# Optimization experiments

Measured on AMD Instinct MI355X. Metric: run time of the kernel, lower is better.

## Reference

```python
import jax, jax.numpy as jnp
import numpy as np

N, E, G = 100000, 1600000, 512
F_IN, H = 226, 128
BN_EPS = 1e-5

def _params(key):
    ks = jax.random.split(key, 34)
    p = {}
    dims = [(F_IN, H), (H, H), (H, H), (H, H)]
    i = 0
    for l, (din, dout) in enumerate(dims, start=1):
        p[f"W{l}a"] = jax.random.normal(ks[i], (din, dout), jnp.float32) * 0.05; i += 1
        p[f"b{l}a"] = jnp.zeros((dout,), jnp.float32)
        p[f"g{l}"] = jnp.ones((dout,), jnp.float32)
        p[f"be{l}"] = jnp.zeros((dout,), jnp.float32)
        p[f"rm{l}"] = jax.random.normal(ks[i], (dout,), jnp.float32) * 0.01; i += 1
        p[f"rv{l}"] = jnp.ones((dout,), jnp.float32)
        p[f"W{l}b"] = jax.random.normal(ks[i], (dout, dout), jnp.float32) * 0.05; i += 1
        p[f"b{l}b"] = jnp.zeros((dout,), jnp.float32)
    p["Wl"] = jax.random.normal(ks[i], (H, 1), jnp.float32) * 0.05
    p["bl"] = jnp.zeros((1,), jnp.float32)
    return p

def setup_inputs() -> dict:
    key = jax.random.key(0)
    k1, k2, k3, kp = jax.random.split(key, 4)
    inp = {
        "x": jax.random.normal(k1, (N, F_IN), jnp.float32),
        "edge_index": jax.random.randint(k2, (2, E), 0, N, jnp.int64),
        "batch": jnp.sort(jax.random.randint(k3, (N,), 0, G, jnp.int64)),
    }
    inp.update(_params(kp))
    return inp

def _gin_layer(x, src, dst, Wa, ba, g, be, rm, rv, Wb, bb):
    # GINConv (eps=0): mlp(x + sum_{j in N(i)} x_j)
    agg = jax.ops.segment_sum(x[src], dst, num_segments=N)  # [N,H] scatter-add
    h = (x + agg) @ Wa + ba
    h = g * (h - rm) * jax.lax.rsqrt(rv + BN_EPS) + be  # eval-mode BatchNorm1d
    h = jax.nn.relu(h)
    h = h @ Wb + bb
    return jax.nn.relu(h)  # outer F.relu after conv

def reference(x, edge_index, batch,
              W1a, b1a, g1, be1, rm1, rv1, W1b, b1b,
              W2a, b2a, g2, be2, rm2, rv2, W2b, b2b,
              W3a, b3a, g3, be3, rm3, rv3, W3b, b3b,
              W4a, b4a, g4, be4, rm4, rv4, W4b, b4b,
              Wl, bl):
    src, dst = edge_index[0], edge_index[1]
    h = _gin_layer(x, src, dst, W1a, b1a, g1, be1, rm1, rv1, W1b, b1b)
    h = _gin_layer(h, src, dst, W2a, b2a, g2, be2, rm2, rv2, W2b, b2b)
    h = _gin_layer(h, src, dst, W3a, b3a, g3, be3, rm3, rv3, W3b, b3b)
    h = _gin_layer(h, src, dst, W4a, b4a, g4, be4, rm4, rv4, W4b, b4b)
    # global mean pool over graphs
    sums = jax.ops.segment_sum(h, batch, num_segments=G)          # [G,H]
    cnts = jax.ops.segment_sum(jnp.ones((N,), h.dtype), batch, num_segments=G)
    pooled = sums / jnp.maximum(cnts, 1.0)[:, None]
    return pooled @ Wl + bl  # [G,1]
```

## Files before the change

### kernel.cpp

```cpp
#include <hip/hip_runtime.h>

#define NN 100000
#define NE 1600000
#define NG 512
#define FIN 226
#define HD 128
#define BN_EPS 1e-5f
#define NBUK 196
#define BCAP 10016

typedef __attribute__((ext_vector_type(8))) __bf16 bf16x8;
typedef __attribute__((ext_vector_type(8))) short short8;
typedef __attribute__((ext_vector_type(8))) unsigned short ushort8;
typedef __attribute__((ext_vector_type(4))) float f32x4;
typedef __attribute__((ext_vector_type(2))) float f32x2;

#define BC(x) __builtin_bit_cast(bf16x8, x)

__device__ inline unsigned short f2bf(float v) {
  unsigned u = __builtin_bit_cast(unsigned, v);
  return (unsigned short)((u + 0x7FFFu + ((u >> 16) & 1u)) >> 16);
}
__device__ inline float bf2f(unsigned short b) {
  return __builtin_bit_cast(float, (unsigned)b << 16);
}

__global__ __launch_bounds__(256) void k_bucket(const int* __restrict__ src,
                                                const int* __restrict__ dst,
                                                int* __restrict__ gcur,
                                                unsigned* __restrict__ pairs) {
  __shared__ int sd[4096];
  __shared__ int ss[4096];
  __shared__ int sh[NBUK];
  __shared__ int sexcl[NBUK];
  __shared__ int scur[NBUK];
  __shared__ int sbase[NBUK];
  __shared__ int wsum[4];
  const int tid = threadIdx.x;
  const int i0 = blockIdx.x * 4096;
  #pragma unroll
  for (int j = 0; j < 16; ++j) {
    int e = i0 + j * 256 + tid;
    sd[j * 256 + tid] = (e < NE) ? __builtin_nontemporal_load(dst + e) : -1;
    ss[j * 256 + tid] = (e < NE) ? __builtin_nontemporal_load(src + e) : 0;
  }
  if (tid < NBUK) sh[tid] = 0;
  __syncthreads();
  #pragma unroll
  for (int j = 0; j < 16; ++j) {
    int d = sd[j * 256 + tid];
    if (d >= 0) atomicAdd(&sh[d >> 9], 1);
  }
  __syncthreads();
  {
    int v = (tid < NBUK) ? sh[tid] : 0;
    int lane = tid & 63, w = tid >> 6;
    int incl = v;
    #pragma unroll
    for (int o = 1; o < 64; o <<= 1) {
      int u = __shfl_up(incl, o);
      if (lane >= o) incl += u;
    }
    if (lane == 63) wsum[w] = incl;
    __syncthreads();
    int off = 0;
    for (int k = 0; k < w; ++k) off += wsum[k];
    if (tid < NBUK) {
      int ex = off + incl - v;
      sexcl[tid] = ex;
      scur[tid] = ex;
      sbase[tid] = (v > 0) ? atomicAdd(&gcur[tid], v) : 0;
    }
  }
  __syncthreads();
  #pragma unroll
  for (int j = 0; j < 16; ++j) {
    int d = sd[j * 256 + tid];
    if (d >= 0) {
      int b = d >> 9;
      int lp = atomicAdd(&scur[b], 1);
      unsigned pk = ((unsigned)(d & 511) << 17) | (unsigned)ss[j * 256 + tid];
      pairs[(size_t)b * BCAP + sbase[b] + (lp - sexcl[b])] = pk;
    }
  }
}

__global__ __launch_bounds__(256) void k_bscan(const int* __restrict__ gcur,
                                               int* __restrict__ bucket_base,
                                               int* __restrict__ row_ptr) {
  __shared__ int wsum[4];
  const int tid = threadIdx.x;
  int v = (tid < NBUK) ? gcur[tid] : 0;
  int lane = tid & 63, w = tid >> 6;
  int incl = v;
  #pragma unroll
  for (int o = 1; o < 64; o <<= 1) {
    int u = __shfl_up(incl, o);
    if (lane >= o) incl += u;
  }
  if (lane == 63) wsum[w] = incl;
  __syncthreads();
  int off = 0;
  for (int k = 0; k < w; ++k) off += wsum[k];
  if (tid < NBUK) bucket_base[tid] = off + incl - v;
  if (tid == 0) row_ptr[NN] = NE;
}

__global__ __launch_bounds__(256) void k_pass2(const unsigned* __restrict__ pairs,
                                               const int* __restrict__ gcur,
                                               const int* __restrict__ bucket_base,
                                               int* __restrict__ row_ptr,
                                               int* __restrict__ col_idx) {
  __shared__ unsigned spk[BCAP];
  __shared__ int h[512];
  __shared__ int cur[512];
  __shared__ int wsum[4];
  const int b = blockIdx.x;
  const int tid = threadIdx.x;
  const int cnt = gcur[b];
  const int base = bucket_base[b];
  for (int i = tid; i < cnt; i += 256) spk[i] = pairs[(size_t)b * BCAP + i];
  h[tid] = 0; h[tid + 256] = 0;
  __syncthreads();
  for (int i = tid; i < cnt; i += 256) atomicAdd(&h[spk[i] >> 17], 1);
  __syncthreads();
  int c0 = h[2 * tid], c1 = h[2 * tid + 1];
  {
    int v = c0 + c1;
    int lane = tid & 63, w = tid >> 6;
    int incl = v;
    #pragma unroll
    for (int o = 1; o < 64; o <<= 1) {
      int u = __shfl_up(incl, o);
      if (lane >= o) incl += u;
    }
    if (lane == 63) wsum[w] = incl;
    __syncthreads();
    int off = 0;
    for (int k = 0; k < w; ++k) off += wsum[k];
    int e0 = off + incl - v;
    int e1 = e0 + c0;
    int node0 = b * 512 + 2 * tid;
    if (node0 < NN) row_ptr[node0] = base + e0;
    if (node0 + 1 < NN) row_ptr[node0 + 1] = base + e1;
    cur[2 * tid] = e0;
    cur[2 * tid + 1] = e1;
  }
  __syncthreads();
  for (int i = tid; i < cnt; i += 256) {
    unsigned pk = spk[i];
    int dl = pk >> 17;
    int p = atomicAdd(&cur[dl], 1);
    col_idx[base + p] = (int)(pk & 0x1FFFFu);
  }
}

struct PrepArgs {
  const float* W[9];
  const float* g[9];
  const float* rv[9];
  unsigned short* out[9];
  int k0[9];
  int K[9];
  const float* ba[4];
  const float* gg[4];
  const float* be[4];
  const float* rm[4];
  const float* rvv[4];
  float* bout;
};

__global__ __launch_bounds__(256) void k_prep(PrepArgs a) {
  int id = blockIdx.x * 256 + threadIdx.x;
  if (id < 9 * 16384) {
    int chunk = id >> 14;
    int r = id & 16383;
    int kk = r >> 7;
    int n = r & 127;
    float s = a.g[chunk] ? a.g[chunk][n] * rsqrtf(a.rv[chunk][n] + BN_EPS) : 1.f;
    int kg = a.k0[chunk] + kk;
    float v = (kg < a.K[chunk]) ? a.W[chunk][(size_t)kg * HD + n] * s : 0.f;
    unsigned short hb = f2bf(v);
    unsigned short lb = f2bf(v - bf2f(hb));
    int idx = n * 128 + (kk ^ ((n & 7) << 3));
    a.out[chunk][idx] = hb;
    a.out[chunk][16384 + idx] = lb;
  } else {
    int t = id - 9 * 16384;
    if (t < 512) {
      int l = t >> 7, c = t & 127;
      float s = a.gg[l][c] * rsqrtf(a.rvv[l][c] + BN_EPS);
      a.bout[l * 128 + c] = a.ba[l][c] * s + a.be[l][c] - a.rm[l][c] * s;
    }
  }
}

__global__ __launch_bounds__(256) void k_mgemm1(const float* __restrict__ A,
                                                const unsigned short* __restrict__ Wz,
                                                unsigned short* __restrict__ out,
                                                int K, int nchunks) {
  __shared__ unsigned short sW[32768];
  const int tid = threadIdx.x;
  const int wv = tid >> 6, ln = tid & 63;
  const int l15 = ln & 15, l4 = ln >> 4;
  const int m0 = blockIdx.x * 128 + wv * 32;
  f32x4 acc[2][8] = {};
  const int sw = (l15 & 7) << 3;
  int kofs[4];
  #pragma unroll
  for (int ks = 0; ks < 4; ++ks) kofs[ks] = (((ks * 32 + l4 * 8) ^ sw)) + l15 * 128;

  for (int c = 0; c < nchunks; ++c) {
    {
      const ushort8* src = (const ushort8*)(Wz + (size_t)c * 32768);
      ushort8* dst = (ushort8*)sW;
      #pragma unroll
      for (int i = 0; i < 16; ++i) dst[tid + i * 256] = src[tid + i * 256];
    }
    __syncthreads();
    const int kc = c * 128;
    #pragma unroll
    for (int ks = 0; ks < 4; ++ks) {
      const int kbase = kc + ks * 32 + l4 * 8;
      const bool tail = (kc + ks * 32 + 32) > K;
      short8 ah[2], al[2];
      #pragma unroll
      for (int mf = 0; mf < 2; ++mf) {
        const int row = m0 + mf * 16 + l15;
        float v[8];
        if (row < NN && !tail) {
          const f32x2* ap = (const f32x2*)(A + (size_t)row * K + kbase);
          #pragma unroll
          for (int q = 0; q < 4; ++q) {
            f32x2 t = __builtin_nontemporal_load(ap + q);
            v[2 * q] = t[0]; v[2 * q + 1] = t[1];
          }
        } else if (row < NN) {
          #pragma unroll
          for (int j = 0; j < 8; ++j) {
            int k = kbase + j;
            v[j] = (k < K) ? A[(size_t)row * K + k] : 0.f;
          }
        } else {
          #pragma unroll
          for (int j = 0; j < 8; ++j) v[j] = 0.f;
        }
        #pragma unroll
        for (int j = 0; j < 8; ++j) {
          unsigned short hb = f2bf(v[j]);
          ah[mf][j] = (short)hb;
          al[mf][j] = (short)f2bf(v[j] - bf2f(hb));
        }
      }
      #pragma unroll
      for (int n = 0; n < 8; ++n) {
        const int idx = n * 2048 + kofs[ks];
        short8 bh = *(const short8*)&sW[idx];
        short8 bl = *(const short8*)&sW[idx + 16384];
        #pragma unroll
        for (int mf = 0; mf < 2; ++mf) {
          acc[mf][n] = __builtin_amdgcn_mfma_f32_16x16x32_bf16(BC(ah[mf]), BC(bh), acc[mf][n], 0, 0, 0);
          acc[mf][n] = __builtin_amdgcn_mfma_f32_16x16x32_bf16(BC(ah[mf]), BC(bl), acc[mf][n], 0, 0, 0);
          acc[mf][n] = __builtin_amdgcn_mfma_f32_16x16x32_bf16(BC(al[mf]), BC(bh), acc[mf][n], 0, 0, 0);
        }
      }
    }
    __syncthreads();
  }
  #pragma unroll
  for (int mf = 0; mf < 2; ++mf) {
    #pragma unroll
    for (int n = 0; n < 8; ++n) {
      const int col = n * 16 + l15;
      #pragma unroll
      for (int r = 0; r < 4; ++r) {
        const int row = m0 + mf * 16 + l4 * 4 + r;
        if (row < NN) out[(size_t)row * HD + col] = f2bf(acc[mf][n][r]);
      }
    }
  }
}

template <int BIAS, int RELU>
__global__ __launch_bounds__(256) void k_mgemmB(const unsigned short* __restrict__ A,
                                                const unsigned short* __restrict__ Wz,
                                                const float* __restrict__ bias,
                                                unsigned short* __restrict__ out) {
  __shared__ unsigned short sW[32768];
  const int tid = threadIdx.x;
  const int wv = tid >> 6, ln = tid & 63;
  const int l15 = ln & 15, l4 = ln >> 4;
  const int m0 = blockIdx.x * 128 + wv * 32;
  f32x4 acc[2][8] = {};
  const int sw = (l15 & 7) << 3;
  {
    const ushort8* src = (const ushort8*)Wz;
    ushort8* dst = (ushort8*)sW;
    #pragma unroll
    for (int i = 0; i < 16; ++i) dst[tid + i * 256] = src[tid + i * 256];
  }
  __syncthreads();
  #pragma unroll
  for (int ks = 0; ks < 4; ++ks) {
    const int kbase = ks * 32 + l4 * 8;
    short8 a[2];
    #pragma unroll
    for (int mf = 0; mf < 2; ++mf) {
      const int row = m0 + mf * 16 + l15;
      if (row < NN) a[mf] = *(const short8*)(A + (size_t)row * HD + kbase);
      else a[mf] = short8{0, 0, 0, 0, 0, 0, 0, 0};
    }
    const int kof = (kbase ^ sw) + l15 * 128;
    #pragma unroll
    for (int n = 0; n < 8; ++n) {
      const int idx = n * 2048 + kof;
      short8 bh = *(const short8*)&sW[idx];
      short8 bl = *(const short8*)&sW[idx + 16384];
      #pragma unroll
      for (int mf = 0; mf < 2; ++mf) {
        acc[mf][n] = __builtin_amdgcn_mfma_f32_16x16x32_bf16(BC(a[mf]), BC(bh), acc[mf][n], 0, 0, 0);
        acc[mf][n] = __builtin_amdgcn_mfma_f32_16x16x32_bf16(BC(a[mf]), BC(bl), acc[mf][n], 0, 0, 0);
      }
    }
  }
  #pragma unroll
  for (int mf = 0; mf < 2; ++mf) {
    #pragma unroll
    for (int n = 0; n < 8; ++n) {
      const int col = n * 16 + l15;
      float bv = BIAS ? bias[col] : 0.f;
      #pragma unroll
      for (int r = 0; r < 4; ++r) {
        const int row = m0 + mf * 16 + l4 * 4 + r;
        if (row < NN) {
          float o = acc[mf][n][r] + bv;
          if (RELU) o = fmaxf(o, 0.f);
          out[(size_t)row * HD + col] = f2bf(o);
        }
      }
    }
  }
}

__global__ __launch_bounds__(256) void k_fused(const unsigned short* __restrict__ H,
                                               const unsigned short* __restrict__ Wzb,
                                               const float* __restrict__ bb,
                                               const unsigned short* __restrict__ Wza,
                                               unsigned short* __restrict__ Yout) {
  __shared__ unsigned short sB[16384];
  __shared__ unsigned short sA2[16384];
  __shared__ unsigned short sX[8192];
  const int tid = threadIdx.x;
  const int wv = tid >> 6, ln = tid & 63;
  const int l15 = ln & 15, l4 = ln >> 4;
  const int m0 = blockIdx.x * 128 + wv * 32;
  const int sw = (l15 & 7) << 3;
  f32x4 acc2[2][8] = {};

  short8 a[2][4];
  #pragma unroll
  for (int mf = 0; mf < 2; ++mf) {
    const int row = m0 + mf * 16 + l15;
    #pragma unroll
    for (int ks = 0; ks < 4; ++ks) {
      if (row < NN) a[mf][ks] = *(const short8*)(H + (size_t)row * HD + ks * 32 + l4 * 8);
      else a[mf][ks] = short8{0, 0, 0, 0, 0, 0, 0, 0};
    }
  }

  #pragma unroll 1
  for (int p = 0; p < 2; ++p) {
    {
      ushort8* d = (ushort8*)sB;
      const ushort8* s1 = (const ushort8*)(Wzb + p * 8192);
      const ushort8* s2 = (const ushort8*)(Wzb + 16384 + p * 8192);
      #pragma unroll
      for (int i = 0; i < 4; ++i) d[tid + i * 256] = s1[tid + i * 256];
      #pragma unroll
      for (int i = 0; i < 4; ++i) d[1024 + tid + i * 256] = s2[tid + i * 256];
    }
    {
      ushort8* d2 = (ushort8*)sA2;
      const ushort8* sa = (const ushort8*)Wza;
      #pragma unroll
      for (int i = 0; i < 4; ++i) {
        int idx = tid + i * 256;
        int n = idx >> 3, q8 = idx & 7;
        d2[idx] = sa[n * 16 + p * 8 + q8];
      }
      #pragma unroll
      for (int i = 0; i < 4; ++i) {
        int idx = tid + i * 256;
        int n = idx >> 3, q8 = idx & 7;
        d2[1024 + idx] = sa[2048 + n * 16 + p * 8 + q8];
      }
    }
    __syncthreads();

    f32x4 acc1[2][4] = {};
    #pragma unroll
    for (int ks = 0; ks < 4; ++ks) {
      const int kof = (ks * 32 + l4 * 8) ^ sw;
      #pragma unroll
      for (int nf = 0; nf < 4; ++nf) {
        const int idx = (nf * 16 + l15) * 128 + kof;
        short8 bh = *(const short8*)&sB[idx];
        short8 bl = *(const short8*)&sB[8192 + idx];
        #pragma unroll
        for (int mf = 0; mf < 2; ++mf) {
          acc1[mf][nf] = __builtin_amdgcn_mfma_f32_16x16x32_bf16(BC(a[mf][ks]), BC(bh), acc1[mf][nf], 0, 0, 0);
          acc1[mf][nf] = __builtin_amdgcn_mfma_f32_16x16x32_bf16(BC(a[mf][ks]), BC(bl), acc1[mf][nf], 0, 0, 0);
        }
      }
    }
    #pragma unroll
    for (int mf = 0; mf < 2; ++mf) {
      #pragma unroll
      for (int nf = 0; nf < 4; ++nf) {
        const int colL = nf * 16 + l15;
        const float bv = bb[p * 64 + colL];
        #pragma unroll
        for (int r = 0; r < 4; ++r) {
          const int rowL = wv * 32 + mf * 16 + l4 * 4 + r;
          sX[rowL * 64 + (colL ^ ((rowL & 7) << 3))] = f2bf(fmaxf(acc1[mf][nf][r] + bv, 0.f));
        }
      }
    }
    #pragma unroll
    for (int ks2 = 0; ks2 < 2; ++ks2) {
      const int xkof = (ks2 * 32 + l4 * 8) ^ sw;
      short8 xf[2];
      #pragma unroll
      for (int mf = 0; mf < 2; ++mf) {
        const int rowL = wv * 32 + mf * 16 + l15;
        xf[mf] = *(const short8*)&sX[rowL * 64 + xkof];
      }
      #pragma unroll
      for (int nf = 0; nf < 8; ++nf) {
        const int idx = (nf * 16 + l15) * 64 + xkof;
        short8 wh = *(const short8*)&sA2[idx];
        short8 wl = *(const short8*)&sA2[8192 + idx];
        #pragma unroll
        for (int mf = 0; mf < 2; ++mf) {
          acc2[mf][nf] = __builtin_amdgcn_mfma_f32_16x16x32_bf16(BC(xf[mf]), BC(wh), acc2[mf][nf], 0, 0, 0);
          acc2[mf][nf] = __builtin_amdgcn_mfma_f32_16x16x32_bf16(BC(xf[mf]), BC(wl), acc2[mf][nf], 0, 0, 0);
        }
      }
    }
    __syncthreads();
  }
  #pragma unroll
  for (int mf = 0; mf < 2; ++mf) {
    #pragma unroll
    for (int n = 0; n < 8; ++n) {
      const int col = n * 16 + l15;
      #pragma unroll
      for (int r = 0; r < 4; ++r) {
        const int row = m0 + mf * 16 + l4 * 4 + r;
        if (row < NN) Yout[(size_t)row * HD + col] = f2bf(acc2[mf][n][r]);
      }
    }
  }
}

__global__ __launch_bounds__(256) void k_agg(const unsigned short* __restrict__ y,
                                             const int* __restrict__ row_ptr,
                                             const int* __restrict__ col_idx,
                                             const float* __restrict__ bias,
                                             unsigned short* __restrict__ h) {
  const int node = blockIdx.x * 4 + (threadIdx.x >> 6);
  const int ln = threadIdx.x & 63;
  const int l15 = ln & 15, grp = ln >> 4;
  if (node >= NN) return;
  float acc[8] = {};
  const int beg = row_ptr[node], end = row_ptr[node + 1];
  int e = beg;
  for (; e + 8 <= end; e += 8) {
    const int s0 = __builtin_nontemporal_load(col_idx + e + grp);
    const int s1 = __builtin_nontemporal_load(col_idx + e + 4 + grp);
    const ushort8 v0 = *(const ushort8*)(y + (size_t)s0 * HD + l15 * 8);
    const ushort8 v1 = *(const ushort8*)(y + (size_t)s1 * HD + l15 * 8);
    #pragma unroll
    for (int j = 0; j < 8; ++j)
      acc[j] += bf2f((unsigned short)v0[j]) + bf2f((unsigned short)v1[j]);
  }
  if (e + 4 <= end) {
    const int s0 = __builtin_nontemporal_load(col_idx + e + grp);
    const ushort8 v0 = *(const ushort8*)(y + (size_t)s0 * HD + l15 * 8);
    #pragma unroll
    for (int j = 0; j < 8; ++j) acc[j] += bf2f((unsigned short)v0[j]);
    e += 4;
  }
  if (e + grp < end) {
    const int s0 = col_idx[e + grp];
    const ushort8 v0 = *(const ushort8*)(y + (size_t)s0 * HD + l15 * 8);
    #pragma unroll
    for (int j = 0; j < 8; ++j) acc[j] += bf2f((unsigned short)v0[j]);
  }
  #pragma unroll
  for (int j = 0; j < 8; ++j) {
    acc[j] += __shfl_xor(acc[j], 16);
    acc[j] += __shfl_xor(acc[j], 32);
  }
  const ushort8 sv = *(const ushort8*)(y + (size_t)node * HD + l15 * 8);
  const f32x4* b4 = (const f32x4*)(bias + l15 * 8);
  const f32x4 b0 = b4[0], b1 = b4[1];
  ushort8 o;
  #pragma unroll
  for (int j = 0; j < 8; ++j) {
    const float bj = (j < 4) ? b0[j] : b1[j - 4];
    o[j] = (unsigned short)f2bf(fmaxf(acc[j] + bf2f((unsigned short)sv[j]) + bj, 0.f));
  }
  if (grp == 0) *(ushort8*)(h + (size_t)node * HD + l15 * 8) = o;
}

__global__ __launch_bounds__(256) void k_pool2(const unsigned short* __restrict__ h,
                                               const int* __restrict__ batch,
                                               const float* __restrict__ Wl,
                                               float* __restrict__ sums,
                                               float* __restrict__ cnts) {
  __shared__ float sb[NG];
  __shared__ int sc[NG];
  const int tid = threadIdx.x;
  for (int i = tid; i < NG; i += 256) { sb[i] = 0.f; sc[i] = 0; }
  __syncthreads();
  const int wv = tid >> 6, ln = tid & 63;
  const float2 w2 = reinterpret_cast<const float2*>(Wl)[ln];
  #pragma unroll 1
  for (int i = 0; i < 16; ++i) {
    const int node = blockIdx.x * 64 + wv * 16 + i;
    if (node < NN) {
      const ushort2 hv = reinterpret_cast<const ushort2*>(h)[(size_t)node * 64 + ln];
      float d = bf2f(hv.x) * w2.x + bf2f(hv.y) * w2.y;
      #pragma unroll
      for (int off = 32; off > 0; off >>= 1) d += __shfl_down(d, off);
      if (ln == 0) {
        const int g = batch[node];
        atomicAdd(&sb[g], d);
        atomicAdd(&sc[g], 1);
      }
    }
  }
  __syncthreads();
  for (int i = tid; i < NG; i += 256)
    if (sc[i]) { atomicAdd(&sums[i], sb[i]); atomicAdd(&cnts[i], (float)sc[i]); }
}

__global__ void k_final(const float* __restrict__ sums, const float* __restrict__ cnts,
                        const float* __restrict__ bl, float* __restrict__ out) {
  int g = blockIdx.x * 256 + threadIdx.x;
  if (g < NG) out[g] = sums[g] / fmaxf(cnts[g], 1.f) + bl[0];
}

extern "C" void kernel_launch(void* const* d_in, const int* in_sizes, int n_in,
                              void* d_out, int out_size, void* d_ws, size_t ws_size,
                              hipStream_t stream) {
  const float* x = (const float*)d_in[0];
  const int* edges = (const int*)d_in[1];
  const int* batch = (const int*)d_in[2];
  const int* e_src = edges;
  const int* e_dst = edges + NE;
  const float* Wl = (const float*)d_in[35];
  const float* bl = (const float*)d_in[36];
  float* out = (float*)d_out;
  auto P = [&](int l, int which) -> const float* {
    return (const float*)d_in[3 + (l - 1) * 8 + which];
  };

  char* ws = (char*)d_ws;
  size_t off = 0;
  auto take = [&](size_t bytes) -> void* {
    void* p = ws + off;
    off = (off + bytes + 255) & ~(size_t)255;
    return p;
  };
  unsigned short* Y = (unsigned short*)take((size_t)NN * HD * 2);
  unsigned short* H = (unsigned short*)take((size_t)NN * HD * 2);
  unsigned short* X = (unsigned short*)take((size_t)NN * HD * 2);
  int* row_ptr = (int*)take((size_t)(NN + 1) * 4);
  int* col_idx = (int*)take((size_t)NE * 4);
  unsigned* pairs = (unsigned*)take((size_t)NBUK * BCAP * 4);
  int* gcur = (int*)take((size_t)NBUK * 4);
  int* bucket_base = (int*)take((size_t)NBUK * 4);
  unsigned short* Wza[4];
  unsigned short* Wzb[4];
  Wza[0] = (unsigned short*)take((size_t)2 * 32768 * 2);
  for (int l = 1; l < 4; ++l) Wza[l] = (unsigned short*)take((size_t)32768 * 2);
  for (int l = 0; l < 4; ++l) Wzb[l] = (unsigned short*)take((size_t)32768 * 2);
  float* bf = (float*)take((size_t)4 * HD * 4);
  float* psum = (float*)take((size_t)NG * 4 * 2);
  float* pcnt = psum + NG;

  hipMemsetAsync(gcur, 0, (size_t)NBUK * 4, stream);
  k_bucket<<<(NE + 4095) / 4096, 256, 0, stream>>>(e_src, e_dst, gcur, pairs);
  k_bscan<<<1, 256, 0, stream>>>(gcur, bucket_base, row_ptr);
  k_pass2<<<NBUK, 256, 0, stream>>>(pairs, gcur, bucket_base, row_ptr, col_idx);

  PrepArgs pa;
  for (int c = 0; c < 9; ++c) {
    if (c < 2) { pa.W[c] = P(1, 0); pa.g[c] = P(1, 2); pa.rv[c] = P(1, 5);
                 pa.out[c] = Wza[0] + c * 32768; pa.k0[c] = c * 128; pa.K[c] = FIN; }
    else if (c < 5) { int l = c - 1; pa.W[c] = P(l + 1, 0); pa.g[c] = P(l + 1, 2);
                      pa.rv[c] = P(l + 1, 5); pa.out[c] = Wza[l]; pa.k0[c] = 0; pa.K[c] = HD; }
    else { int l = c - 5; pa.W[c] = P(l + 1, 6); pa.g[c] = nullptr; pa.rv[c] = nullptr;
           pa.out[c] = Wzb[l]; pa.k0[c] = 0; pa.K[c] = HD; }
  }
  for (int l = 0; l < 4; ++l) {
    pa.ba[l] = P(l + 1, 1); pa.gg[l] = P(l + 1, 2); pa.be[l] = P(l + 1, 3);
    pa.rm[l] = P(l + 1, 4); pa.rvv[l] = P(l + 1, 5);
  }
  pa.bout = bf;
  k_prep<<<(9 * 16384 + 512 + 255) / 256, 256, 0, stream>>>(pa);

  hipMemsetAsync(psum, 0, (size_t)NG * 8, stream);

  const int gemm_grid = (NN + 127) / 128;
  k_mgemm1<<<gemm_grid, 256, 0, stream>>>(x, Wza[0], Y, FIN, 2);
  for (int l = 1; l <= 3; ++l) {
    k_agg<<<NN / 4, 256, 0, stream>>>(Y, row_ptr, col_idx, bf + (l - 1) * HD, H);
    k_fused<<<gemm_grid, 256, 0, stream>>>(H, Wzb[l - 1], P(l, 7), Wza[l], Y);
  }
  k_agg<<<NN / 4, 256, 0, stream>>>(Y, row_ptr, col_idx, bf + 3 * HD, H);
  k_mgemmB<1, 1><<<gemm_grid, 256, 0, stream>>>(H, Wzb[3], P(4, 7), X);
  k_pool2<<<(NN + 63) / 64, 256, 0, stream>>>(X, batch, Wl, psum, pcnt);
  k_final<<<(NG + 255) / 256, 256, 0, stream>>>(psum, pcnt, bl, out);
}
```

Measured before the change: 533.3 us.

## Fuse neighbor aggregation into GEMM kernels and fold bucket scan into pass2

The separate aggregation kernel is merged into the per-layer fused MLP kernel. Each block gathers its 128 rows' neighbor sums into swizzled shared memory and feeds them straight to the MFMA GEMMs, so the H intermediate never goes to global memory. The last layer also fuses the second GEMM, the ReLU, the dot with Wl and the per-graph pooling into one kernel, and the bucket prefix scan is recomputed inside each pass2 block, removing two launches. The cost is that the gather is less parallel (16 lanes per row rather than a 64-thread wave split across edges), shared memory grows to about 80KB, which may lower occupancy, and Y is ping-ponged between two buffers.

```diff
diff --git a/kernel.cpp b/kernel.cpp
--- a/kernel.cpp
+++ b/kernel.cpp
@@ -85,40 +85,36 @@
   }
 }
 
-__global__ __launch_bounds__(256) void k_bscan(const int* __restrict__ gcur,
-                                               int* __restrict__ bucket_base,
-                                               int* __restrict__ row_ptr) {
-  __shared__ int wsum[4];
-  const int tid = threadIdx.x;
-  int v = (tid < NBUK) ? gcur[tid] : 0;
-  int lane = tid & 63, w = tid >> 6;
-  int incl = v;
-  #pragma unroll
-  for (int o = 1; o < 64; o <<= 1) {
-    int u = __shfl_up(incl, o);
-    if (lane >= o) incl += u;
-  }
-  if (lane == 63) wsum[w] = incl;
-  __syncthreads();
-  int off = 0;
-  for (int k = 0; k < w; ++k) off += wsum[k];
-  if (tid < NBUK) bucket_base[tid] = off + incl - v;
-  if (tid == 0) row_ptr[NN] = NE;
-}
-
 __global__ __launch_bounds__(256) void k_pass2(const unsigned* __restrict__ pairs,
                                                const int* __restrict__ gcur,
-                                               const int* __restrict__ bucket_base,
                                                int* __restrict__ row_ptr,
                                                int* __restrict__ col_idx) {
   __shared__ unsigned spk[BCAP];
   __shared__ int h[512];
   __shared__ int cur[512];
   __shared__ int wsum[4];
+  __shared__ int s_base;
   const int b = blockIdx.x;
   const int tid = threadIdx.x;
+  {
+    int v = (tid < NBUK) ? gcur[tid] : 0;
+    int lane = tid & 63, w = tid >> 6;
+    int incl = v;
+    #pragma unroll
+    for (int o = 1; o < 64; o <<= 1) {
+      int u = __shfl_up(incl, o);
+      if (lane >= o) incl += u;
+    }
+    if (lane == 63) wsum[w] = incl;
+    __syncthreads();
+    int off = 0;
+    for (int k = 0; k < w; ++k) off += wsum[k];
+    if (tid == b) s_base = off + incl - v;
+    if (b == 0 && tid == 0) row_ptr[NN] = NE;
+  }
   const int cnt = gcur[b];
-  const int base = bucket_base[b];
+  __syncthreads();
+  const int base = s_base;
   for (int i = tid; i < cnt; i += 256) spk[i] = pairs[(size_t)b * BCAP + i];
   h[tid] = 0; h[tid + 256] = 0;
   __syncthreads();
@@ -281,93 +277,78 @@
   }
 }
 
-template <int BIAS, int RELU>
-__global__ __launch_bounds__(256) void k_mgemmB(const unsigned short* __restrict__ A,
-                                                const unsigned short* __restrict__ Wz,
-                                                const float* __restrict__ bias,
-                                                unsigned short* __restrict__ out) {
-  __shared__ unsigned short sW[32768];
+__global__ __launch_bounds__(256) void k_aggemm(const unsigned short* __restrict__ Y,
+                                                const int* __restrict__ row_ptr,
+                                                const int* __restrict__ col_idx,
+                                                const float* __restrict__ bias_a,
+                                                const unsigned short* __restrict__ Wzb,
+                                                const float* __restrict__ bb,
+                                                const unsigned short* __restrict__ Wza,
+                                                unsigned short* __restrict__ Yout) {
+  __shared__ __align__(16) char smem[81920];
+  unsigned short* sH = (unsigned short*)smem;
+  unsigned short* sB = (unsigned short*)smem;
+  unsigned short* sA2 = (unsigned short*)(smem + 32768);
+  unsigned short* sX = (unsigned short*)(smem + 65536);
   const int tid = threadIdx.x;
   const int wv = tid >> 6, ln = tid & 63;
-  const int l15 = ln & 15, l4 = ln >> 4;
-  const int m0 = blockIdx.x * 128 + wv * 32;
-  f32x4 acc[2][8] = {};
-  const int sw = (l15 & 7) << 3;
-  {
-    const ushort8* src = (const ushort8*)Wz;
-    ushort8* dst = (ushort8*)sW;
-    #pragma unroll
-    for (int i = 0; i < 16; ++i) dst[tid + i * 256] = src[tid + i * 256];
-  }
-  __syncthreads();
-  #pragma unroll
-  for (int ks = 0; ks < 4; ++ks) {
-    const int kbase = ks * 32 + l4 * 8;
-    short8 a[2];
-    #pragma unroll
-    for (int mf = 0; mf < 2; ++mf) {
-      const int row = m0 + mf * 16 + l15;
-      if (row < NN) a[mf] = *(const short8*)(A + (size_t)row * HD + kbase);
-      else a[mf] = short8{0, 0, 0, 0, 0, 0, 0, 0};
-    }
-    const int kof = (kbase ^ sw) + l15 * 128;
-    #pragma unroll
-    for (int n = 0; n < 8; ++n) {
-      const int idx = n * 2048 + kof;
-      short8 bh = *(const short8*)&sW[idx];
-      short8 bl = *(const short8*)&sW[idx + 16384];
-      #pragma unroll
-      for (int mf = 0; mf < 2; ++mf) {
-        acc[mf][n] = __builtin_amdgcn_mfma_f32_16x16x32_bf16(BC(a[mf]), BC(bh), acc[mf][n], 0, 0, 0);
-        acc[mf][n] = __builtin_amdgcn_mfma_f32_16x16x32_bf16(BC(a[mf]), BC(bl), acc[mf][n], 0, 0, 0);
-      }
-    }
-  }
-  #pragma unroll
-  for (int mf = 0; mf < 2; ++mf) {
-    #pragma unroll
-    for (int n = 0; n < 8; ++n) {
-      const int col = n * 16 + l15;
-      float bv = BIAS ? bias[col] : 0.f;
-      #pragma unroll
-      for (int r = 0; r < 4; ++r) {
-        const int row = m0 + mf * 16 + l4 * 4 + r;
-        if (row < NN) {
-          float o = acc[mf][n][r] + bv;
-          if (RELU) o = fmaxf(o, 0.f);
-          out[(size_t)row * HD + col] = f2bf(o);
-        }
-      }
-    }
-  }
-}
-
-__global__ __launch_bounds__(256) void k_fused(const unsigned short* __restrict__ H,
-                                               const unsigned short* __restrict__ Wzb,
-                                               const float* __restrict__ bb,
-                                               const unsigned short* __restrict__ Wza,
-                                               unsigned short* __restrict__ Yout) {
-  __shared__ unsigned short sB[16384];
-  __shared__ unsigned short sA2[16384];
-  __shared__ unsigned short sX[8192];
-  const int tid = threadIdx.x;
-  const int wv = tid >> 6, ln = tid & 63;
-  const int l15 = ln & 15, l4 = ln >> 4;
+  const int l15 = ln & 15, grp = ln >> 4;
   const int m0 = blockIdx.x * 128 + wv * 32;
   const int sw = (l15 & 7) << 3;
+
+  const f32x4* b4 = (const f32x4*)(bias_a + l15 * 8);
+  const f32x4 ba0 = b4[0], ba1 = b4[1];
+  #pragma unroll 1
+  for (int io = 0; io < 8; ++io) {
+    const int rloc = wv * 32 + io * 4 + grp;
+    const int row = blockIdx.x * 128 + rloc;
+    float acc[8] = {};
+    const bool valid = row < NN;
+    int beg = 0, end = 0;
+    if (valid) { beg = row_ptr[row]; end = row_ptr[row + 1]; }
+    int e = beg;
+    for (; e + 4 <= end; e += 4) {
+      const int s0 = col_idx[e], s1 = col_idx[e + 1];
+      const int s2 = col_idx[e + 2], s3 = col_idx[e + 3];
+      const ushort8 v0 = *(const ushort8*)(Y + (size_t)s0 * HD + l15 * 8);
+      const ushort8 v1 = *(const ushort8*)(Y + (size_t)s1 * HD + l15 * 8);
+      const ushort8 v2 = *(const ushort8*)(Y + (size_t)s2 * HD + l15 * 8);
+      const ushort8 v3 = *(const ushort8*)(Y + (size_t)s3 * HD + l15 * 8);
+      #pragma unroll
+      for (int j = 0; j < 8; ++j)
+        acc[j] += (bf2f((unsigned short)v0[j]) + bf2f((unsigned short)v1[j])) +
+                  (bf2f((unsigned short)v2[j]) + bf2f((unsigned short)v3[j]));
+    }
+    for (; e < end; ++e) {
+      const int s0 = col_idx[e];
+      const ushort8 v0 = *(const ushort8*)(Y + (size_t)s0 * HD + l15 * 8);
+      #pragma unroll
+      for (int j = 0; j < 8; ++j) acc[j] += bf2f((unsigned short)v0[j]);
+    }
+    ushort8 o = {0, 0, 0, 0, 0, 0, 0, 0};
+    if (valid) {
+      const ushort8 sv = *(const ushort8*)(Y + (size_t)row * HD + l15 * 8);
+      #pragma unroll
+      for (int j = 0; j < 8; ++j) {
+        const float bj = (j < 4) ? ba0[j] : ba1[j - 4];
+        o[j] = (unsigned short)f2bf(fmaxf(acc[j] + bf2f((unsigned short)sv[j]) + bj, 0.f));
+      }
+    }
+    *(ushort8*)&sH[rloc * 128 + ((l15 ^ (rloc & 7)) * 8)] = o;
+  }
+  short8 a[2][4];
+  #pragma unroll
+  for (int mf = 0; mf < 2; ++mf) {
+    const int rl = wv * 32 + mf * 16 + l15;
+    #pragma unroll
+    for (int ks = 0; ks < 4; ++ks) {
+      const int chunk = (ks * 4 + grp) ^ (rl & 7);
+      a[mf][ks] = *(const short8*)&sH[rl * 128 + chunk * 8];
+    }
+  }
+  __syncthreads();
+
   f32x4 acc2[2][8] = {};
-
-  short8 a[2][4];
-  #pragma unroll
-  for (int mf = 0; mf < 2; ++mf) {
-    const int row = m0 + mf * 16 + l15;
-    #pragma unroll
-    for (int ks = 0; ks < 4; ++ks) {
-      if (row < NN) a[mf][ks] = *(const short8*)(H + (size_t)row * HD + ks * 32 + l4 * 8);
-      else a[mf][ks] = short8{0, 0, 0, 0, 0, 0, 0, 0};
-    }
-  }
-
   #pragma unroll 1
   for (int p = 0; p < 2; ++p) {
     {
@@ -400,7 +381,7 @@
     f32x4 acc1[2][4] = {};
     #pragma unroll
     for (int ks = 0; ks < 4; ++ks) {
-      const int kof = (ks * 32 + l4 * 8) ^ sw;
+      const int kof = (ks * 32 + grp * 8) ^ sw;
       #pragma unroll
       for (int nf = 0; nf < 4; ++nf) {
         const int idx = (nf * 16 + l15) * 128 + kof;
@@ -421,14 +402,14 @@
         const float bv = bb[p * 64 + colL];
         #pragma unroll
         for (int r = 0; r < 4; ++r) {
-          const int rowL = wv * 32 + mf * 16 + l4 * 4 + r;
+          const int rowL = wv * 32 + mf * 16 + grp * 4 + r;
           sX[rowL * 64 + (colL ^ ((rowL & 7) << 3))] = f2bf(fmaxf(acc1[mf][nf][r] + bv, 0.f));
         }
       }
     }
     #pragma unroll
     for (int ks2 = 0; ks2 < 2; ++ks2) {
-      const int xkof = (ks2 * 32 + l4 * 8) ^ sw;
+      const int xkof = (ks2 * 32 + grp * 8) ^ sw;
       short8 xf[2];
       #pragma unroll
       for (int mf = 0; mf < 2; ++mf) {
@@ -456,88 +437,146 @@
       const int col = n * 16 + l15;
       #pragma unroll
       for (int r = 0; r < 4; ++r) {
-        const int row = m0 + mf * 16 + l4 * 4 + r;
+        const int row = m0 + mf * 16 + grp * 4 + r;
         if (row < NN) Yout[(size_t)row * HD + col] = f2bf(acc2[mf][n][r]);
       }
     }
   }
 }
 
-__global__ __launch_bounds__(256) void k_agg(const unsigned short* __restrict__ y,
-                                             const int* __restrict__ row_ptr,
-                                             const int* __restrict__ col_idx,
-                                             const float* __restrict__ bias,
-                                             unsigned short* __restrict__ h) {
-  const int node = blockIdx.x * 4 + (threadIdx.x >> 6);
-  const int ln = threadIdx.x & 63;
-  const int l15 = ln & 15, grp = ln >> 4;
-  if (node >= NN) return;
-  float acc[8] = {};
-  const int beg = row_ptr[node], end = row_ptr[node + 1];
-  int e = beg;
-  for (; e + 8 <= end; e += 8) {
-    const int s0 = __builtin_nontemporal_load(col_idx + e + grp);
-    const int s1 = __builtin_nontemporal_load(col_idx + e + 4 + grp);
-    const ushort8 v0 = *(const ushort8*)(y + (size_t)s0 * HD + l15 * 8);
-    const ushort8 v1 = *(const ushort8*)(y + (size_t)s1 * HD + l15 * 8);
-    #pragma unroll
-    for (int j = 0; j < 8; ++j)
-      acc[j] += bf2f((unsigned short)v0[j]) + bf2f((unsigned short)v1[j]);
-  }
-  if (e + 4 <= end) {
-    const int s0 = __builtin_nontemporal_load(col_idx + e + grp);
-    const ushort8 v0 = *(const ushort8*)(y + (size_t)s0 * HD + l15 * 8);
-    #pragma unroll
-    for (int j = 0; j < 8; ++j) acc[j] += bf2f((unsigned short)v0[j]);
-    e += 4;
-  }
-  if (e + grp < end) {
-    const int s0 = col_idx[e + grp];
-    const ushort8 v0 = *(const ushort8*)(y + (size_t)s0 * HD + l15 * 8);
-    #pragma unroll
-    for (int j = 0; j < 8; ++j) acc[j] += bf2f((unsigned short)v0[j]);
-  }
-  #pragma unroll
-  for (int j = 0; j < 8; ++j) {
-    acc[j] += __shfl_xor(acc[j], 16);
-    acc[j] += __shfl_xor(acc[j], 32);
-  }
-  const ushort8 sv = *(const ushort8*)(y + (size_t)node * HD + l15 * 8);
-  const f32x4* b4 = (const f32x4*)(bias + l15 * 8);
-  const f32x4 b0 = b4[0], b1 = b4[1];
-  ushort8 o;
-  #pragma unroll
-  for (int j = 0; j < 8; ++j) {
-    const float bj = (j < 4) ? b0[j] : b1[j - 4];
-    o[j] = (unsigned short)f2bf(fmaxf(acc[j] + bf2f((unsigned short)sv[j]) + bj, 0.f));
-  }
-  if (grp == 0) *(ushort8*)(h + (size_t)node * HD + l15 * 8) = o;
-}
-
-__global__ __launch_bounds__(256) void k_pool2(const unsigned short* __restrict__ h,
-                                               const int* __restrict__ batch,
-                                               const float* __restrict__ Wl,
-                                               float* __restrict__ sums,
-                                               float* __restrict__ cnts) {
+__global__ __launch_bounds__(256) void k_aggpool(const unsigned short* __restrict__ Y,
+                                                 const int* __restrict__ row_ptr,
+                                                 const int* __restrict__ col_idx,
+                                                 const float* __restrict__ bias_a,
+                                                 const unsigned short* __restrict__ Wzb,
+                                                 const float* __restrict__ bb,
+                                                 const float* __restrict__ Wl,
+                                                 const int* __restrict__ batch,
+                                                 float* __restrict__ sums,
+                                                 float* __restrict__ cnts) {
+  __shared__ __align__(16) char smem[32768];
+  unsigned short* sH = (unsigned short*)smem;
+  unsigned short* sB = (unsigned short*)smem;
   __shared__ float sb[NG];
   __shared__ int sc[NG];
   const int tid = threadIdx.x;
+  const int wv = tid >> 6, ln = tid & 63;
+  const int l15 = ln & 15, grp = ln >> 4;
+  const int m0 = blockIdx.x * 128 + wv * 32;
+  const int sw = (l15 & 7) << 3;
   for (int i = tid; i < NG; i += 256) { sb[i] = 0.f; sc[i] = 0; }
-  __syncthreads();
-  const int wv = tid >> 6, ln = tid & 63;
-  const float2 w2 = reinterpret_cast<const float2*>(Wl)[ln];
+
+  const f32x4* b4 = (const f32x4*)(bias_a + l15 * 8);
+  const f32x4 ba0 = b4[0], ba1 = b4[1];
   #pragma unroll 1
-  for (int i = 0; i < 16; ++i) {
-    const int node = blockIdx.x * 64 + wv * 16 + i;
-    if (node < NN) {
-      const ushort2 hv = reinterpret_cast<const ushort2*>(h)[(size_t)node * 64 + ln];
-      float d = bf2f(hv.x) * w2.x + bf2f(hv.y) * w2.y;
-      #pragma unroll
-      for (int off = 32; off > 0; off >>= 1) d += __shfl_down(d, off);
-      if (ln == 0) {
-        const int g = batch[node];
-        atomicAdd(&sb[g], d);
-        atomicAdd(&sc[g], 1);
+  for (int io = 0; io < 8; ++io) {
+    const int rloc = wv * 32 + io * 4 + grp;
+    const int row = blockIdx.x * 128 + rloc;
+    float acc[8] = {};
+    const bool valid = row < NN;
+    int beg = 0, end = 0;
+    if (valid) { beg = row_ptr[row]; end = row_ptr[row + 1]; }
+    int e = beg;
+    for (; e + 4 <= end; e += 4) {
+      const int s0 = col_idx[e], s1 = col_idx[e + 1];
+      const int s2 = col_idx[e + 2], s3 = col_idx[e + 3];
+      const ushort8 v0 = *(const ushort8*)(Y + (size_t)s0 * HD + l15 * 8);
+      const ushort8 v1 = *(const ushort8*)(Y + (size_t)s1 * HD + l15 * 8);
+      const ushort8 v2 = *(const ushort8*)(Y + (size_t)s2 * HD + l15 * 8);
+      const ushort8 v3 = *(const ushort8*)(Y + (size_t)s3 * HD + l15 * 8);
+      #pragma unroll
+      for (int j = 0; j < 8; ++j)
+        acc[j] += (bf2f((unsigned short)v0[j]) + bf2f((unsigned short)v1[j])) +
+                  (bf2f((unsigned short)v2[j]) + bf2f((unsigned short)v3[j]));
+    }
+    for (; e < end; ++e) {
+      const int s0 = col_idx[e];
+      const ushort8 v0 = *(const ushort8*)(Y + (size_t)s0 * HD + l15 * 8);
+      #pragma unroll
+      for (int j = 0; j < 8; ++j) acc[j] += bf2f((unsigned short)v0[j]);
+    }
+    ushort8 o = {0, 0, 0, 0, 0, 0, 0, 0};
+    if (valid) {
+      const ushort8 sv = *(const ushort8*)(Y + (size_t)row * HD + l15 * 8);
+      #pragma unroll
+      for (int j = 0; j < 8; ++j) {
+        const float bj = (j < 4) ? ba0[j] : ba1[j - 4];
+        o[j] = (unsigned short)f2bf(fmaxf(acc[j] + bf2f((unsigned short)sv[j]) + bj, 0.f));
+      }
+    }
+    *(ushort8*)&sH[rloc * 128 + ((l15 ^ (rloc & 7)) * 8)] = o;
+  }
+  short8 a[2][4];
+  #pragma unroll
+  for (int mf = 0; mf < 2; ++mf) {
+    const int rl = wv * 32 + mf * 16 + l15;
+    #pragma unroll
+    for (int ks = 0; ks < 4; ++ks) {
+      const int chunk = (ks * 4 + grp) ^ (rl & 7);
+      a[mf][ks] = *(const short8*)&sH[rl * 128 + chunk * 8];
+    }
+  }
+  __syncthreads();
+
+  float pdot[2][4] = {};
+  #pragma unroll 1
+  for (int p = 0; p < 2; ++p) {
+    {
+      ushort8* d = (ushort8*)sB;
+      const ushort8* s1 = (const ushort8*)(Wzb + p * 8192);
+      const ushort8* s2 = (const ushort8*)(Wzb + 16384 + p * 8192);
+      #pragma unroll
+      for (int i = 0; i < 4; ++i) d[tid + i * 256] = s1[tid + i * 256];
+      #pragma unroll
+      for (int i = 0; i < 4; ++i) d[1024 + tid + i * 256] = s2[tid + i * 256];
+    }
+    __syncthreads();
+    f32x4 acc1[2][4] = {};
+    #pragma unroll
+    for (int ks = 0; ks < 4; ++ks) {
+      const int kof = (ks * 32 + grp * 8) ^ sw;
+      #pragma unroll
+      for (int nf = 0; nf < 4; ++nf) {
+        const int idx = (nf * 16 + l15) * 128 + kof;
+        short8 bh = *(const short8*)&sB[idx];
+        short8 bl = *(const short8*)&sB[8192 + idx];
+        #pragma unroll
+        for (int mf = 0; mf < 2; ++mf) {
+          acc1[mf][nf] = __builtin_amdgcn_mfma_f32_16x16x32_bf16(BC(a[mf][ks]), BC(bh), acc1[mf][nf], 0, 0, 0);
+          acc1[mf][nf] = __builtin_amdgcn_mfma_f32_16x16x32_bf16(BC(a[mf][ks]), BC(bl), acc1[mf][nf], 0, 0, 0);
+        }
+      }
+    }
+    #pragma unroll
+    for (int mf = 0; mf < 2; ++mf) {
+      #pragma unroll
+      for (int nf = 0; nf < 4; ++nf) {
+        const int col = p * 64 + nf * 16 + l15;
+        const float bv = bb[col];
+        const float wl = Wl[col];
+        #pragma unroll
+        for (int r = 0; r < 4; ++r)
+          pdot[mf][r] += fmaxf(acc1[mf][nf][r] + bv, 0.f) * wl;
+      }
+    }
+    __syncthreads();
+  }
+  #pragma unroll
+  for (int mf = 0; mf < 2; ++mf) {
+    #pragma unroll
+    for (int r = 0; r < 4; ++r) {
+      float d = pdot[mf][r];
+      d += __shfl_xor(d, 1);
+      d += __shfl_xor(d, 2);
+      d += __shfl_xor(d, 4);
+      d += __shfl_xor(d, 8);
+      if (l15 == 0) {
+        const int row = m0 + mf * 16 + grp * 4 + r;
+        if (row < NN) {
+          const int g = batch[row];
+          atomicAdd(&sb[g], d);
+          atomicAdd(&sc[g], 1);
+        }
       }
     }
   }
@@ -574,14 +613,12 @@
     off = (off + bytes + 255) & ~(size_t)255;
     return p;
   };
-  unsigned short* Y = (unsigned short*)take((size_t)NN * HD * 2);
-  unsigned short* H = (unsigned short*)take((size_t)NN * HD * 2);
-  unsigned short* X = (unsigned short*)take((size_t)NN * HD * 2);
+  unsigned short* Y0 = (unsigned short*)take((size_t)NN * HD * 2);
+  unsigned short* Y1 = (unsigned short*)take((size_t)NN * HD * 2);
   int* row_ptr = (int*)take((size_t)(NN + 1) * 4);
   int* col_idx = (int*)take((size_t)NE * 4);
   unsigned* pairs = (unsigned*)take((size_t)NBUK * BCAP * 4);
   int* gcur = (int*)take((size_t)NBUK * 4);
-  int* bucket_base = (int*)take((size_t)NBUK * 4);
   unsigned short* Wza[4];
   unsigned short* Wzb[4];
   Wza[0] = (unsigned short*)take((size_t)2 * 32768 * 2);
@@ -593,8 +630,7 @@
 
   hipMemsetAsync(gcur, 0, (size_t)NBUK * 4, stream);
   k_bucket<<<(NE + 4095) / 4096, 256, 0, stream>>>(e_src, e_dst, gcur, pairs);
-  k_bscan<<<1, 256, 0, stream>>>(gcur, bucket_base, row_ptr);
-  k_pass2<<<NBUK, 256, 0, stream>>>(pairs, gcur, bucket_base, row_ptr, col_idx);
+  k_pass2<<<NBUK, 256, 0, stream>>>(pairs, gcur, row_ptr, col_idx);
 
   PrepArgs pa;
   for (int c = 0; c < 9; ++c) {
@@ -614,14 +650,16 @@
 
   hipMemsetAsync(psum, 0, (size_t)NG * 8, stream);
 
-  const int gemm_grid = (NN + 127) / 128;
-  k_mgemm1<<<gemm_grid, 256, 0, stream>>>(x, Wza[0], Y, FIN, 2);
+  const int grid = (NN + 127) / 128;
+  k_mgemm1<<<grid, 256, 0, stream>>>(x, Wza[0], Y0, FIN, 2);
+  unsigned short* cur = Y0;
+  unsigned short* nxt = Y1;
   for (int l = 1; l <= 3; ++l) {
-    k_agg<<<NN / 4, 256, 0, stream>>>(Y, row_ptr, col_idx, bf + (l - 1) * HD, H);
-    k_fused<<<gemm_grid, 256, 0, stream>>>(H, Wzb[l - 1], P(l, 7), Wza[l], Y);
-  }
-  k_agg<<<NN / 4, 256, 0, stream>>>(Y, row_ptr, col_idx, bf + 3 * HD, H);
-  k_mgemmB<1, 1><<<gemm_grid, 256, 0, stream>>>(H, Wzb[3], P(4, 7), X);
-  k_pool2<<<(NN + 63) / 64, 256, 0, stream>>>(X, batch, Wl, psum, pcnt);
+    k_aggemm<<<grid, 256, 0, stream>>>(cur, row_ptr, col_idx, bf + (l - 1) * HD,
+                                       Wzb[l - 1], P(l, 7), Wza[l], nxt);
+    unsigned short* t = cur; cur = nxt; nxt = t;
+  }
+  k_aggpool<<<grid, 256, 0, stream>>>(cur, row_ptr, col_idx, bf + 3 * HD,
+                                      Wzb[3], P(4, 7), Wl, batch, psum, pcnt);
   k_final<<<(NG + 255) / 256, 256, 0, stream>>>(psum, pcnt, bl, out);
 }
```

Result: slower. 578.9 us (+8.6%).
